# Performance work log

Hardware: AMD Instinct MI355X
Metric: run time of the kernel (lower is better)

The kernel has to match this reference:

```python
import jax, jax.numpy as jnp
import numpy as np

N, D, H = 2048, 1024, 16
DH = D // H
SCALE = 1.0 / DH ** 0.5


def setup_inputs() -> dict:
    key = jax.random.key(0)
    k0, k1, k2 = jax.random.split(key, 3)
    lim_qkv = 1.0 / np.sqrt(D)
    lim_proj = 1.0 / np.sqrt(D)
    return {
        "x": jax.random.normal(k0, (N, D), dtype=jnp.float32),
        "w_qkv": jax.random.uniform(k1, (3 * D, D), jnp.float32, -lim_qkv, lim_qkv),
        "b_qkv": jnp.zeros((3 * D,), jnp.float32),
        "w_proj": jax.random.uniform(k2, (D, D), jnp.float32, -lim_proj, lim_proj),
        "b_proj": jnp.zeros((D,), jnp.float32),
    }


def reference(x, w_qkv, b_qkv, w_proj, b_proj) -> jnp.ndarray:
    # qkv linear: (N, D) -> (N, 3D)
    qkv = x @ w_qkv.T + b_qkv
    q, k, v = jnp.split(qkv, 3, axis=-1)
    # (N, D) -> (H, N, Dh)
    def _heads(a):
        return a.reshape(N, H, DH).transpose(1, 0, 2)
    q, k, v = map(_heads, (q, k, v))
    # full NxN scores per head (faithful to original einsum+softmax)
    attn = jax.nn.softmax(jnp.einsum('hnd,hmd->hnm', q * SCALE, k), axis=-1)
    out = jnp.einsum('hnm,hmd->hnd', attn, v)          # (H, N, Dh)
    out = out.transpose(1, 0, 2).reshape(N, D)
    return out @ w_proj.T + b_proj
```

## Files before the change

kernel.cpp:

```cpp
#include <hip/hip_runtime.h>
#include <hip/hip_bf16.h>
#include <cstdint>

typedef unsigned short u16;
typedef __attribute__((ext_vector_type(8)))  short bf16x8;
typedef __attribute__((ext_vector_type(4)))  float f32x4;
typedef __attribute__((ext_vector_type(16))) float f32x16;
typedef __attribute__((ext_vector_type(2)))  unsigned int uint2v;

#define N_TOK   2048
#define DMODEL  1024
#define NHEAD   16
#define DHEAD   64
#define QKV_N   3072
#define QK_LD   2048
#define NSPLIT  4
#define KV_PER  (N_TOK / NSPLIT)
#define C1_LOG2 0.1803368801111244f
#define M0_BASE 4.0f

__device__ __forceinline__ u16 f2b(float f) {
  uint32_t u = __float_as_uint(f);
  u += 0x7FFFu + ((u >> 16) & 1u);
  return (u16)(u >> 16);
}
__device__ __forceinline__ float b2f(u16 b) {
  return __uint_as_float(((uint32_t)b) << 16);
}
__device__ __forceinline__ float fexp2(float x) { return __builtin_amdgcn_exp2f(x); }

__device__ __forceinline__ uint32_t cvtpk(float lo, float hi) {
  uint32_t r;
  asm("v_cvt_pk_bf16_f32 %0, %1, %2" : "=v"(r) : "v"(lo), "v"(hi));
  return r;
}

__device__ __forceinline__ float xsum32(float x) {
  uint2v d = __builtin_amdgcn_permlane32_swap(__float_as_uint(x), __float_as_uint(x), false, false);
  return __uint_as_float(d.x) + __uint_as_float(d.y);
}

__device__ __forceinline__ void gload_lds16(const void* g, void* l) {
  __builtin_amdgcn_global_load_lds(
      (const __attribute__((address_space(1))) void*)g,
      (__attribute__((address_space(3))) void*)l,
      16, 0, 0);
}

__global__ __launch_bounds__(256)
void cvt_all(const float* __restrict__ x, const float* __restrict__ wq,
             const float* __restrict__ wp,
             u16* __restrict__ xb, u16* __restrict__ wqb, u16* __restrict__ wpb) {
  const int i = blockIdx.x * 256 + threadIdx.x;
  const int NX = (N_TOK * DMODEL) / 4;
  const int NQ = (3 * DMODEL * DMODEL) / 4;
  const float4* src; u16* dst; int j;
  if (i < NX)            { src = (const float4*)x;  dst = xb;  j = i; }
  else if (i < NX + NQ)  { src = (const float4*)wq; dst = wqb; j = i - NX; }
  else                   { src = (const float4*)wp; dst = wpb; j = i - NX - NQ; }
  const float4 v = src[j];
  ushort4 pk;
  pk.x = f2b(v.x); pk.y = f2b(v.y); pk.z = f2b(v.z); pk.w = f2b(v.w);
  ((ushort4*)dst)[j] = pk;
}

template<bool OUT_F32, bool FUSE_VT, int MI, int NI>
__global__ __launch_bounds__(256, 2)
void gemm_nt(const u16* __restrict__ A, const u16* __restrict__ B,
             const float* __restrict__ bias, void* __restrict__ Cv,
             u16* __restrict__ vtg, int ldc, int K) {
  __shared__ alignas(16) u16 As[2][MI * 32 * 64];
  __shared__ alignas(16) u16 Bs[2][NI * 32 * 64];
  const int tid = threadIdx.x;
  const int w = tid >> 6, l = tid & 63;
  const int lo = l & 15, hi = l >> 4;
  const int wr = w >> 1, wc = w & 1;
  const int bm = blockIdx.y * (MI * 32), bn = blockIdx.x * (NI * 32);
  f32x4 acc[MI][NI] = {};
  const int NK = K >> 6;

  auto stage = [&](int kb, int bufi) {
#pragma unroll
    for (int i = 0; i < MI; ++i) {
      const int c = w * (MI * 64) + i * 64 + l;
      const int r = c >> 3, gs = (c ^ r) & 7;
      gload_lds16(A + (size_t)(bm + r) * K + kb + gs * 8, (char*)As[bufi] + (size_t)c * 16);
    }
#pragma unroll
    for (int i = 0; i < NI; ++i) {
      const int c = w * (NI * 64) + i * 64 + l;
      const int r = c >> 3, gs = (c ^ r) & 7;
      gload_lds16(B + (size_t)(bn + r) * K + kb + gs * 8, (char*)Bs[bufi] + (size_t)c * 16);
    }
  };

  stage(0, 0);
  int buf = 0;
  for (int t = 0; t < NK; ++t) {
    if (t + 1 < NK) {
      stage((t + 1) * 64, buf ^ 1);
      if constexpr (MI + NI == 7)      asm volatile("s_waitcnt vmcnt(7)" ::: "memory");
      else if constexpr (MI + NI == 6) asm volatile("s_waitcnt vmcnt(6)" ::: "memory");
      else if constexpr (MI + NI == 4) asm volatile("s_waitcnt vmcnt(4)" ::: "memory");
      else                             asm volatile("s_waitcnt vmcnt(8)" ::: "memory");
    } else {
      asm volatile("s_waitcnt vmcnt(0)" ::: "memory");
    }
    __builtin_amdgcn_s_barrier();

    bf16x8 af[MI][2], bfr[NI][2];
#pragma unroll
    for (int mi = 0; mi < MI; ++mi)
#pragma unroll
      for (int ks = 0; ks < 2; ++ks) {
        const int ra = wr * (MI * 16) + mi * 16 + lo;
        af[mi][ks] = *(const bf16x8*)((const char*)As[buf] + ra * 128 +
                                      (((ks * 4 + hi) ^ (ra & 7)) << 4));
      }
#pragma unroll
    for (int ni = 0; ni < NI; ++ni)
#pragma unroll
      for (int ks = 0; ks < 2; ++ks) {
        const int rb = wc * (NI * 16) + ni * 16 + lo;
        bfr[ni][ks] = *(const bf16x8*)((const char*)Bs[buf] + rb * 128 +
                                       (((ks * 4 + hi) ^ (rb & 7)) << 4));
      }
#pragma unroll
    for (int mi = 0; mi < MI; ++mi)
#pragma unroll
      for (int ni = 0; ni < NI; ++ni)
#pragma unroll
        for (int ks = 0; ks < 2; ++ks)
          acc[mi][ni] = __builtin_amdgcn_mfma_f32_16x16x32_bf16(af[mi][ks], bfr[ni][ks], acc[mi][ni], 0, 0, 0);

    __builtin_amdgcn_s_barrier();
    buf ^= 1;
  }

#pragma unroll
  for (int mi = 0; mi < MI; ++mi)
#pragma unroll
    for (int ni = 0; ni < NI; ++ni) {
      const int col = bn + wc * (NI * 16) + ni * 16 + lo;
      const float bv = bias[col];
      if constexpr (FUSE_VT) {
        if (col >= 2 * DMODEL) {
          const int row0 = bm + wr * (MI * 16) + mi * 16 + hi * 4;
          ushort4 pk;
          pk.x = f2b(acc[mi][ni][0] + bv);
          pk.y = f2b(acc[mi][ni][1] + bv);
          pk.z = f2b(acc[mi][ni][2] + bv);
          pk.w = f2b(acc[mi][ni][3] + bv);
          *(ushort4*)(vtg + (size_t)(col - 2 * DMODEL) * N_TOK + row0) = pk;
        } else {
          const float sc = (col < DMODEL) ? C1_LOG2 : 1.0f;
#pragma unroll
          for (int j = 0; j < 4; ++j) {
            const int row = bm + wr * (MI * 16) + mi * 16 + hi * 4 + j;
            ((u16*)Cv)[(size_t)row * QK_LD + col] = f2b((acc[mi][ni][j] + bv) * sc);
          }
        }
      } else {
#pragma unroll
        for (int j = 0; j < 4; ++j) {
          const int row = bm + wr * (MI * 16) + mi * 16 + hi * 4 + j;
          const float v = acc[mi][ni][j] + bv;
          if constexpr (OUT_F32) ((float*)Cv)[(size_t)row * ldc + col] = v;
          else                   ((u16*)Cv)[(size_t)row * ldc + col] = f2b(v);
        }
      }
    }
}

#define FRAG(BASE, ROW, SLOT) \
  (*(const bf16x8*)((const char*)(BASE) + (ROW) * 128 + ((((SLOT) ^ ((ROW) & 7))) << 4)))

#define SOFTPACK(SA, SB, PFR, LS) do {                                          \
    float tsum_ = 0.f;                                                          \
    _Pragma("unroll")                                                           \
    for (int ks = 0; ks < 4; ++ks) {                                            \
      float q_[8];                                                              \
      _Pragma("unroll")                                                         \
      for (int j = 0; j < 8; ++j) {                                             \
        const int idx = (ks & 1) * 8 + j;                                       \
        q_[j] = fexp2(((ks < 2) ? (SA)[idx] : (SB)[idx]) - M0_BASE);            \
      }                                                                         \
      tsum_ += ((q_[0] + q_[1]) + (q_[2] + q_[3])) + ((q_[4] + q_[5]) + (q_[6] + q_[7])); \
      uint32_t a1 = cvtpk(q_[0], q_[1]);                                        \
      uint32_t a2 = cvtpk(q_[2], q_[3]);                                        \
      uint32_t b1 = cvtpk(q_[4], q_[5]);                                        \
      uint32_t b2 = cvtpk(q_[6], q_[7]);                                        \
      uint2v r1 = __builtin_amdgcn_permlane32_swap(a1, b1, false, false);       \
      uint2v r2 = __builtin_amdgcn_permlane32_swap(a2, b2, false, false);       \
      union { uint32_t u[4]; bf16x8 h; } cv_;                                   \
      cv_.u[0] = r1.x; cv_.u[1] = r2.x; cv_.u[2] = r1.y; cv_.u[3] = r2.y;       \
      (PFR)[ks] = cv_.h;                                                        \
    }                                                                           \
    (LS) += tsum_;                                                              \
  } while (0)

__global__ __launch_bounds__(256, 2)
void attn3(const u16* __restrict__ qkb, const u16* __restrict__ vtg,
           u16* __restrict__ PO, float* __restrict__ lbuf) {
  __shared__ alignas(16) u16 SMEM[4][64 * 64];
  const int tid = threadIdx.x;
  const int w = tid >> 6, l = tid & 63;
  const int lo = l & 31, hi = l >> 5;

  int bid = (int)blockIdx.x;
  bid = (bid & 7) * 64 + (bid >> 3);
  const int h  = bid >> 5;
  const int qb = (bid >> 2) & 7;
  const int z  = bid & 3;
  const int q0w = qb * 256 + w * 64;
  const int kv0 = z * KV_PER;

  bf16x8 qf0[4], qf1[4];
  {
    const u16* qs0 = qkb + (size_t)(q0w + lo) * QK_LD + h * 64 + hi * 8;
    const u16* qs1 = qkb + (size_t)(q0w + 32 + lo) * QK_LD + h * 64 + hi * 8;
#pragma unroll
    for (int ds = 0; ds < 4; ++ds) { qf0[ds] = *(const bf16x8*)(qs0 + ds * 16);
                                     qf1[ds] = *(const bf16x8*)(qs1 + ds * 16); }
  }

  f32x16 o0 = {}, o1 = {}, o2 = {}, o3 = {};
  float lsum0 = 0.f, lsum1 = 0.f;

#define STAGE(KB, B) do {                                                       \
    _Pragma("unroll")                                                           \
    for (int i_ = 0; i_ < 2; ++i_) {                                            \
      const int c_ = w * 128 + i_ * 64 + l;                                     \
      const int r_ = c_ >> 3;                                                   \
      const int gs_ = (c_ ^ r_) & 7;                                            \
      gload_lds16(qkb + (size_t)((KB) + r_) * QK_LD + DMODEL + h * 64 + gs_ * 8,\
                  (char*)SMEM[B] + (size_t)(w * 128 + i_ * 64) * 16);           \
      gload_lds16(vtg + (size_t)(h * 64 + r_) * N_TOK + (KB) + gs_ * 8,         \
                  (char*)SMEM[2 + (B)] + (size_t)(w * 128 + i_ * 64) * 16);     \
    }                                                                           \
  } while (0)

  STAGE(kv0, 0);
  int buf = 0;
  for (int t = 0; t < KV_PER / 64; ++t) {
    if (t + 1 < KV_PER / 64) {
      STAGE(kv0 + (t + 1) * 64, buf ^ 1);
      asm volatile("s_waitcnt vmcnt(4)" ::: "memory");
    } else {
      asm volatile("s_waitcnt vmcnt(0)" ::: "memory");
    }
    __builtin_amdgcn_s_barrier();

    const u16* Kb = SMEM[buf];
    const u16* Vb = SMEM[2 + buf];

    f32x16 s0 = {}, s1 = {}, s2 = {}, s3 = {};
    __builtin_amdgcn_s_setprio(1);
#pragma unroll
    for (int ds = 0; ds < 4; ++ds) {
      bf16x8 k0 = FRAG(Kb, lo, ds * 2 + hi);
      bf16x8 k1 = FRAG(Kb, 32 + lo, ds * 2 + hi);
      s0 = __builtin_amdgcn_mfma_f32_32x32x16_bf16(k0, qf0[ds], s0, 0, 0, 0);
      s1 = __builtin_amdgcn_mfma_f32_32x32x16_bf16(k1, qf0[ds], s1, 0, 0, 0);
      s2 = __builtin_amdgcn_mfma_f32_32x32x16_bf16(k0, qf1[ds], s2, 0, 0, 0);
      s3 = __builtin_amdgcn_mfma_f32_32x32x16_bf16(k1, qf1[ds], s3, 0, 0, 0);
    }
    __builtin_amdgcn_s_setprio(0);

    bf16x8 pfr0[4], pfr1[4];
    SOFTPACK(s0, s1, pfr0, lsum0);
    SOFTPACK(s2, s3, pfr1, lsum1);

    __builtin_amdgcn_s_setprio(1);
#pragma unroll
    for (int ks = 0; ks < 4; ++ks) {
      bf16x8 v0 = FRAG(Vb, lo, ks * 2 + hi);
      bf16x8 v1 = FRAG(Vb, 32 + lo, ks * 2 + hi);
      o0 = __builtin_amdgcn_mfma_f32_32x32x16_bf16(v0, pfr0[ks], o0, 0, 0, 0);
      o1 = __builtin_amdgcn_mfma_f32_32x32x16_bf16(v1, pfr0[ks], o1, 0, 0, 0);
      o2 = __builtin_amdgcn_mfma_f32_32x32x16_bf16(v0, pfr1[ks], o2, 0, 0, 0);
      o3 = __builtin_amdgcn_mfma_f32_32x32x16_bf16(v1, pfr1[ks], o3, 0, 0, 0);
    }
    __builtin_amdgcn_s_setprio(0);

    __builtin_amdgcn_s_barrier();
    buf ^= 1;
  }
#undef STAGE

  lsum0 = xsum32(lsum0);
  lsum1 = xsum32(lsum1);

  u16* Ow = ((u16*)SMEM) + w * 4096;
  const float inv0 = 1.0f / lsum0;
  const float inv1 = 1.0f / lsum1;
#pragma unroll
  for (int r = 0; r < 16; ++r) {
    const int crow = (r & 3) + 8 * (r >> 2) + 4 * hi;
    const int c0 = crow, c1 = 32 + crow;
    const int s0i = ((c0 >> 3) ^ (lo & 7)) << 3, s1i = ((c1 >> 3) ^ (lo & 7)) << 3;
    Ow[lo * 64 + s0i + (c0 & 7)] = f2b(o0[r] * inv0);
    Ow[lo * 64 + s1i + (c1 & 7)] = f2b(o1[r] * inv0);
    Ow[(32 + lo) * 64 + s0i + (c0 & 7)] = f2b(o2[r] * inv1);
    Ow[(32 + lo) * 64 + s1i + (c1 & 7)] = f2b(o3[r] * inv1);
  }
  if (hi == 0) {
    lbuf[((size_t)z * NHEAD + h) * N_TOK + q0w + lo] = lsum0;
    lbuf[((size_t)z * NHEAD + h) * N_TOK + q0w + 32 + lo] = lsum1;
  }
  asm volatile("s_waitcnt lgkmcnt(0)" ::: "memory");
  __builtin_amdgcn_sched_barrier(0);
  u16* pobase = PO + (((size_t)z * NHEAD + h) * N_TOK + q0w) * DHEAD;
#pragma unroll
  for (int i = 0; i < 8; ++i) {
    const int c = i * 64 + l;
    const int rr = c >> 3, sl = c & 7;
    bf16x8 v = *(const bf16x8*)(Ow + rr * 64 + sl * 8);
    const int cs = sl ^ (rr & 7);
    *(bf16x8*)(pobase + (size_t)rr * DHEAD + cs * 8) = v;
  }
}

__global__ __launch_bounds__(256)
void combine(const u16* __restrict__ PO, const float* __restrict__ lbuf,
             u16* __restrict__ attb) {
  const int idx = blockIdx.x * 256 + threadIdx.x;
  const int row = idx >> 3;
  const int c8  = (idx & 7) * 8;
  const int h = row >> 11;
  const int q = row & (N_TOK - 1);

  float wsum = 0.f, acc8[8] = {};
#pragma unroll
  for (int zz = 0; zz < NSPLIT; ++zz) {
    const float wz = lbuf[((size_t)zz * NHEAD + h) * N_TOK + q];
    wsum += wz;
    bf16x8 po = *(const bf16x8*)(PO + (((size_t)zz * NHEAD + h) * N_TOK + q) * DHEAD + c8);
#pragma unroll
    for (int j = 0; j < 8; ++j) acc8[j] += wz * b2f((u16)po[j]);
  }
  const float invw = 1.0f / wsum;
  union { u16 s[8]; bf16x8 h8; } ov;
#pragma unroll
  for (int j = 0; j < 8; ++j) ov.s[j] = f2b(acc8[j] * invw);
  *(bf16x8*)(attb + (size_t)q * DMODEL + h * 64 + c8) = ov.h8;
}

extern "C" void kernel_launch(void* const* d_in, const int* in_sizes, int n_in,
                              void* d_out, int out_size, void* d_ws, size_t ws_size,
                              hipStream_t stream) {
  const float* x      = (const float*)d_in[0];
  const float* w_qkv  = (const float*)d_in[1];
  const float* b_qkv  = (const float*)d_in[2];
  const float* w_proj = (const float*)d_in[3];
  const float* b_proj = (const float*)d_in[4];
  float* out = (float*)d_out;

  char* ws = (char*)d_ws;
  u16*    xb     = (u16*)(ws + (0u  << 20));
  u16*    wqkvb  = (u16*)(ws + (8u  << 20));
  u16*    wprojb = (u16*)(ws + (16u << 20));
  u16*    qkb    = (u16*)(ws + (24u << 20));
  u16*    vtg    = (u16*)(ws + (40u << 20));
  u16*    PO     = (u16*)(ws + (48u << 20));
  float*  lbuf   = (float*)(ws + (64u << 20));
  u16*    attb   = (u16*)(ws + (66u << 20));
  if (ws_size < (80u << 20)) return;

  cvt_all<<<6144, 256, 0, stream>>>(x, w_qkv, w_proj, xb, wqkvb, wprojb);

  gemm_nt<false, true, 4, 3><<<dim3(QKV_N / 96, N_TOK / 128), 256, 0, stream>>>(
      xb, wqkvb, b_qkv, (void*)qkb, vtg, QK_LD, DMODEL);

  attn3<<<8 * NHEAD * NSPLIT, 256, 0, stream>>>(qkb, vtg, PO, lbuf);

  combine<<<(N_TOK * NHEAD * 8) / 256, 256, 0, stream>>>(PO, lbuf, attb);

  gemm_nt<true, false, 4, 2><<<dim3(DMODEL / 64, N_TOK / 128), 256, 0, stream>>>(
      attb, wprojb, b_proj, (void*)out, nullptr, DMODEL, DMODEL);
}
```

Measured before the change: 75.67 us.

## Load GEMM A operand directly into registers and shrink projection tile

```diff
diff --git a/kernel.cpp b/kernel.cpp
--- a/kernel.cpp
+++ b/kernel.cpp
@@ -69,7 +69,6 @@
 void gemm_nt(const u16* __restrict__ A, const u16* __restrict__ B,
              const float* __restrict__ bias, void* __restrict__ Cv,
              u16* __restrict__ vtg, int ldc, int K) {
-  __shared__ alignas(16) u16 As[2][MI * 32 * 64];
   __shared__ alignas(16) u16 Bs[2][NI * 32 * 64];
   const int tid = threadIdx.x;
   const int w = tid >> 6, l = tid & 63;
@@ -79,13 +78,9 @@
   f32x4 acc[MI][NI] = {};
   const int NK = K >> 6;
 
-  auto stage = [&](int kb, int bufi) {
-#pragma unroll
-    for (int i = 0; i < MI; ++i) {
-      const int c = w * (MI * 64) + i * 64 + l;
-      const int r = c >> 3, gs = (c ^ r) & 7;
-      gload_lds16(A + (size_t)(bm + r) * K + kb + gs * 8, (char*)As[bufi] + (size_t)c * 16);
-    }
+  const u16* aptr = A + (size_t)(bm + wr * (MI * 16) + lo) * K + hi * 8;
+
+  auto stageB = [&](int kb, int bufi) {
 #pragma unroll
     for (int i = 0; i < NI; ++i) {
       const int c = w * (NI * 64) + i * 64 + l;
@@ -93,36 +88,21 @@
       gload_lds16(B + (size_t)(bn + r) * K + kb + gs * 8, (char*)Bs[bufi] + (size_t)c * 16);
     }
   };
-
-  stage(0, 0);
-  int buf = 0;
-  for (int t = 0; t < NK; ++t) {
-    if (t + 1 < NK) {
-      stage((t + 1) * 64, buf ^ 1);
-      if constexpr (MI + NI == 7)      asm volatile("s_waitcnt vmcnt(7)" ::: "memory");
-      else if constexpr (MI + NI == 6) asm volatile("s_waitcnt vmcnt(6)" ::: "memory");
-      else if constexpr (MI + NI == 4) asm volatile("s_waitcnt vmcnt(4)" ::: "memory");
-      else                             asm volatile("s_waitcnt vmcnt(8)" ::: "memory");
-    } else {
-      asm volatile("s_waitcnt vmcnt(0)" ::: "memory");
-    }
-    __builtin_amdgcn_s_barrier();
-
-    bf16x8 af[MI][2], bfr[NI][2];
+  auto loadA = [&](int kb, bf16x8 (&dst)[MI][2]) {
 #pragma unroll
     for (int mi = 0; mi < MI; ++mi)
 #pragma unroll
-      for (int ks = 0; ks < 2; ++ks) {
-        const int ra = wr * (MI * 16) + mi * 16 + lo;
-        af[mi][ks] = *(const bf16x8*)((const char*)As[buf] + ra * 128 +
-                                      (((ks * 4 + hi) ^ (ra & 7)) << 4));
-      }
+      for (int ks = 0; ks < 2; ++ks)
+        dst[mi][ks] = *(const bf16x8*)(aptr + (size_t)(mi * 16) * K + kb + ks * 32);
+  };
+  auto compute = [&](const bf16x8 (&af)[MI][2], const u16* Bbuf) {
+    bf16x8 bfr[NI][2];
 #pragma unroll
     for (int ni = 0; ni < NI; ++ni)
 #pragma unroll
       for (int ks = 0; ks < 2; ++ks) {
         const int rb = wc * (NI * 16) + ni * 16 + lo;
-        bfr[ni][ks] = *(const bf16x8*)((const char*)Bs[buf] + rb * 128 +
+        bfr[ni][ks] = *(const bf16x8*)((const char*)Bbuf + rb * 128 +
                                        (((ks * 4 + hi) ^ (rb & 7)) << 4));
       }
 #pragma unroll
@@ -132,10 +112,33 @@
 #pragma unroll
         for (int ks = 0; ks < 2; ++ks)
           acc[mi][ni] = __builtin_amdgcn_mfma_f32_16x16x32_bf16(af[mi][ks], bfr[ni][ks], acc[mi][ni], 0, 0, 0);
-
+  };
+
+#define GEMM_VC() do {                                                          \
+    if constexpr (NI + 2 * MI == 11)     asm volatile("s_waitcnt vmcnt(11)" ::: "memory"); \
+    else if constexpr (NI + 2 * MI == 6) asm volatile("s_waitcnt vmcnt(6)"  ::: "memory"); \
+    else                                 asm volatile("s_waitcnt vmcnt(8)"  ::: "memory"); \
+  } while (0)
+
+  bf16x8 afA[MI][2], afB[MI][2];
+  stageB(0, 0);
+  loadA(0, afA);
+  int buf = 0;
+  for (int t = 0; t < NK; t += 2) {
+    if (t + 1 < NK) { stageB((t + 1) * 64, buf ^ 1); loadA((t + 1) * 64, afB); GEMM_VC(); }
+    else            { asm volatile("s_waitcnt vmcnt(0)" ::: "memory"); }
+    __builtin_amdgcn_s_barrier();
+    compute(afA, Bs[buf]);
     __builtin_amdgcn_s_barrier();
     buf ^= 1;
-  }
+    if (t + 2 < NK) { stageB((t + 2) * 64, buf ^ 1); loadA((t + 2) * 64, afA); GEMM_VC(); }
+    else            { asm volatile("s_waitcnt vmcnt(0)" ::: "memory"); }
+    __builtin_amdgcn_s_barrier();
+    compute(afB, Bs[buf]);
+    __builtin_amdgcn_s_barrier();
+    buf ^= 1;
+  }
+#undef GEMM_VC
 
 #pragma unroll
   for (int mi = 0; mi < MI; ++mi)
@@ -376,6 +379,6 @@
 
   combine<<<(N_TOK * NHEAD * 8) / 256, 256, 0, stream>>>(PO, lbuf, attb);
 
-  gemm_nt<true, false, 4, 2><<<dim3(DMODEL / 64, N_TOK / 128), 256, 0, stream>>>(
+  gemm_nt<true, false, 2, 2><<<dim3(DMODEL / 64, N_TOK / 64), 256, 0, stream>>>(
       attb, wprojb, b_proj, (void*)out, nullptr, DMODEL, DMODEL);
 }
```

Result: slower. 96.85 us (+28.0%).
